# Kernel tuning notes

Measured on AMD Instinct MI355X. Metric: run time of the kernel, lower is better.

The kernel has to match this reference:

```python
import jax, jax.numpy as jnp
import numpy as np

N_NODES = 100000
N_EDGES = 1600000
IN_CH, HID, EMB = 128, 64, 32


def _glorot(key, shape):
    lim = np.sqrt(6.0 / (shape[0] + shape[1])).astype(np.float32)
    return jax.random.uniform(key, shape, jnp.float32, -lim, lim)


def setup_inputs() -> dict:
    key = jax.random.key(0)
    ks = jax.random.split(key, 5)
    x = jax.random.normal(ks[0], (N_NODES, IN_CH), dtype=jnp.float32)
    edges = jax.random.randint(ks[1], (2, N_EDGES), 0, N_NODES)
    W1 = _glorot(ks[2], (IN_CH, HID)); b1 = jnp.zeros((HID,), jnp.float32)
    W2 = _glorot(ks[3], (HID, EMB)); b2 = jnp.zeros((EMB,), jnp.float32)
    W3 = _glorot(ks[4], (HID, EMB)); b3 = jnp.zeros((EMB,), jnp.float32)
    return {"x": x, "edges": edges, "W1": W1, "b1": b1,
            "W2": W2, "b2": b2, "W3": W3, "b3": b3}


def reference(x, edges, W1, b1, W2, b2, W3, b3):
    N = x.shape[0]
    # GCNConv default: add self-loops, symmetric D^-1/2 A D^-1/2 normalization
    loop = jnp.arange(N, dtype=edges.dtype)
    src = jnp.concatenate([edges[0], loop])  # [E+N] message sources
    dst = jnp.concatenate([edges[1], loop])  # [E+N] message targets
    deg = jax.ops.segment_sum(jnp.ones_like(dst, dtype=x.dtype), dst, num_segments=N)
    dinv = jnp.where(deg > 0, jax.lax.rsqrt(deg), 0.0)
    norm = dinv[src] * dinv[dst]  # [E+N], cached across the three convs (cached=True)

    def gcn(h, W, b):
        h = h @ W                                  # [N, out]
        msg = h[src] * norm[:, None]               # gather + edge scale
        return jax.ops.segment_sum(msg, dst, num_segments=N) + b  # scatter-add

    h = jax.nn.relu(gcn(x, W1, b1))
    return gcn(h, W2, b2), gcn(h, W3, b3)
```

## Files before the change

kernel.cpp:

```cpp
#include <hip/hip_runtime.h>

#define NN 100000
#define NE 1600000
#define NB 391
#define CHUNK 4096
#define NCHUNK 391

__device__ inline unsigned short f2bf(float f) {
    unsigned int u = __float_as_uint(f);
    unsigned int r = u + 0x7fffu + ((u >> 16) & 1u);
    return (unsigned short)(r >> 16);
}
__device__ inline float bf_lo(unsigned int u) { return __uint_as_float(u << 16); }
__device__ inline float bf_hi(unsigned int u) { return __uint_as_float(u & 0xffff0000u); }

__global__ __launch_bounds__(256) void k_hist(const int* __restrict__ dst,
                                              int* __restrict__ bhist) {
    __shared__ int lh[NB];
    int t = threadIdx.x;
    for (int i = t; i < NB; i += 256) lh[i] = 0;
    __syncthreads();
    for (int e = blockIdx.x * 256 + t; e < NE; e += 256 * 256)
        atomicAdd(&lh[dst[e] >> 8], 1);
    __syncthreads();
    for (int i = t; i < NB; i += 256)
        if (lh[i]) atomicAdd(&bhist[i], lh[i]);
}

__global__ __launch_bounds__(256) void k_scanb(const int* __restrict__ bhist,
                                               int* __restrict__ boff,
                                               int* __restrict__ bcur) {
    __shared__ int sh[256];
    int t = threadIdx.x;
    int base = t * 2;
    int v0 = (base + 0 < NB) ? bhist[base + 0] : 0;
    int v1 = (base + 1 < NB) ? bhist[base + 1] : 0;
    int tsum = v0 + v1;
    sh[t] = tsum;
    __syncthreads();
    for (int d = 1; d < 256; d <<= 1) {
        int x = (t >= d) ? sh[t - d] : 0;
        __syncthreads();
        sh[t] += x;
        __syncthreads();
    }
    int excl = sh[t] - tsum;
    if (base + 0 < NB) { boff[base + 0] = excl;      bcur[base + 0] = excl; }
    if (base + 1 < NB) { boff[base + 1] = excl + v0; bcur[base + 1] = excl + v0; }
    if (t == 255) boff[NB] = sh[255];
}

__global__ __launch_bounds__(512) void k_bscatter(const int* __restrict__ src,
                                                  const int* __restrict__ dst,
                                                  int* __restrict__ bcur,
                                                  unsigned int* __restrict__ pairs) {
    __shared__ int lh[NB];
    __shared__ int lbase[NB];
    int t = threadIdx.x;
    int e0 = blockIdx.x * CHUNK;
    int e1 = min(e0 + CHUNK, NE);
    for (int i = t; i < NB; i += 512) lh[i] = 0;
    __syncthreads();
    for (int e = e0 + t; e < e1; e += 512)
        atomicAdd(&lh[dst[e] >> 8], 1);
    __syncthreads();
    int rot = (int)((blockIdx.x * 97u) % NB);
    for (int i = t; i < NB; i += 512) {
        int ii = i + rot; if (ii >= NB) ii -= NB;
        int h = lh[ii];
        lbase[ii] = h ? atomicAdd(&bcur[ii], h) : 0;
    }
    __syncthreads();
    for (int i = t; i < NB; i += 512) lh[i] = 0;
    __syncthreads();
    for (int e = e0 + t; e < e1; e += 512) {
        int d = dst[e];
        int b = d >> 8;
        int r = atomicAdd(&lh[b], 1);
        pairs[lbase[b] + r] = (unsigned int)src[e] | ((unsigned int)(d & 255) << 17);
    }
}

__global__ __launch_bounds__(256) void k_fine(const unsigned int* __restrict__ pairs,
                                              const int* __restrict__ boff,
                                              int* __restrict__ csr_off,
                                              int* __restrict__ csr_src,
                                              float* __restrict__ dinv) {
    __shared__ int lcnt[256];
    __shared__ int sc[256];
    __shared__ int lofs[256];
    int t = threadIdx.x;
    int b = blockIdx.x;
    int n0 = b << 8;
    int nnode = min(256, NN - n0);
    int bO = boff[b], bE = boff[b + 1];

    lcnt[t] = 0;
    __syncthreads();
    for (int e = bO + t; e < bE; e += 256)
        atomicAdd(&lcnt[pairs[e] >> 17], 1);
    __syncthreads();
    sc[t] = lcnt[t];
    __syncthreads();
    for (int d = 1; d < 256; d <<= 1) {
        int x = (t >= d) ? sc[t - d] : 0;
        __syncthreads();
        sc[t] += x;
        __syncthreads();
    }
    {
        int excl = sc[t] - lcnt[t];
        lofs[t] = excl;
        if (t < nnode) {
            int n = n0 + t;
            csr_off[n] = bO + excl;
            dinv[n] = rsqrtf(1.0f + (float)lcnt[t]);
        }
        lcnt[t] = 0;
    }
    if (b == NB - 1 && t == 0) csr_off[NN] = NE;
    __syncthreads();
    for (int e = bO + t; e < bE; e += 256) {
        unsigned int w = pairs[e];
        int li = (int)(w >> 17);
        int r = atomicAdd(&lcnt[li], 1);
        csr_src[bO + lofs[li] + r] = (int)(w & 0x1FFFFu);
    }
}

__global__ __launch_bounds__(256) void k_gemm1(const float* __restrict__ x,
                                               const float* __restrict__ W1,
                                               const float* __restrict__ dinv,
                                               unsigned short* __restrict__ t1b) {
    __shared__ float xs[64][132];
    __shared__ float ws[128 * 64];
    const int t = threadIdx.x;
    const int row0 = blockIdx.x * 64;
    const int nrows = min(64, NN - row0);

    #pragma unroll
    for (int i = 0; i < 8; ++i) {
        int f = t + i * 256;
        *(float4*)&ws[f * 4] = ((const float4*)W1)[f];
    }
    #pragma unroll
    for (int i = 0; i < 8; ++i) {
        int f = t + i * 256;
        int r = f >> 5, k4 = f & 31;
        float4 v = make_float4(0.f, 0.f, 0.f, 0.f);
        if (r < nrows) v = ((const float4*)(x + (size_t)(row0 + r) * 128))[k4];
        *(float4*)&xs[r][k4 * 4] = v;
    }
    __syncthreads();

    const int tc = t & 15;
    const int tr = t >> 4;
    float acc[4][4];
    #pragma unroll
    for (int i = 0; i < 4; ++i)
        #pragma unroll
        for (int j = 0; j < 4; ++j) acc[i][j] = 0.f;

    #pragma unroll 4
    for (int k = 0; k < 128; ++k) {
        float4 wv = *(const float4*)&ws[k * 64 + tc * 4];
        #pragma unroll
        for (int i = 0; i < 4; ++i) {
            float xv = xs[tr * 4 + i][k];
            acc[i][0] += xv * wv.x; acc[i][1] += xv * wv.y;
            acc[i][2] += xv * wv.z; acc[i][3] += xv * wv.w;
        }
    }
    #pragma unroll
    for (int i = 0; i < 4; ++i) {
        int r = tr * 4 + i;
        if (r < nrows) {
            float dn = dinv[row0 + r];
            ushort4 o;
            o.x = f2bf(acc[i][0] * dn); o.y = f2bf(acc[i][1] * dn);
            o.z = f2bf(acc[i][2] * dn); o.w = f2bf(acc[i][3] * dn);
            *(ushort4*)&t1b[(size_t)(row0 + r) * 64 + tc * 4] = o;
        }
    }
}

template <bool RELU>
__global__ __launch_bounds__(256) void k_gather8(const int* __restrict__ off,
                                                 const int* __restrict__ csr,
                                                 const float* __restrict__ dinv,
                                                 const unsigned short* __restrict__ hb,
                                                 const float* __restrict__ bias,
                                                 unsigned int* __restrict__ outp) {
    int idx = blockIdx.x * 256 + threadIdx.x;
    int n = idx >> 3;
    if (n >= NN) return;
    int c8 = idx & 7;
    const uint4* h4 = (const uint4*)hb;
    float dn = dinv[n];
    float acc[8];
    {
        uint4 v = h4[(size_t)n * 8 + c8];
        acc[0] = bf_lo(v.x); acc[1] = bf_hi(v.x);
        acc[2] = bf_lo(v.y); acc[3] = bf_hi(v.y);
        acc[4] = bf_lo(v.z); acc[5] = bf_hi(v.z);
        acc[6] = bf_lo(v.w); acc[7] = bf_hi(v.w);
    }
    int b = off[n], e = off[n + 1];
    int i = b;
    if (i < e) {
        int s = csr[i];
        for (++i; i < e; ++i) {
            int sn = csr[i];
            uint4 v = h4[(size_t)s * 8 + c8];
            acc[0] += bf_lo(v.x); acc[1] += bf_hi(v.x);
            acc[2] += bf_lo(v.y); acc[3] += bf_hi(v.y);
            acc[4] += bf_lo(v.z); acc[5] += bf_hi(v.z);
            acc[6] += bf_lo(v.w); acc[7] += bf_hi(v.w);
            s = sn;
        }
        uint4 v = h4[(size_t)s * 8 + c8];
        acc[0] += bf_lo(v.x); acc[1] += bf_hi(v.x);
        acc[2] += bf_lo(v.y); acc[3] += bf_hi(v.y);
        acc[4] += bf_lo(v.z); acc[5] += bf_hi(v.z);
        acc[6] += bf_lo(v.w); acc[7] += bf_hi(v.w);
    }
    float o[8];
    if (RELU) {
        float4 b0 = ((const float4*)bias)[c8 * 2];
        float4 b1 = ((const float4*)bias)[c8 * 2 + 1];
        o[0] = dn * fmaxf(dn * acc[0] + b0.x, 0.f);
        o[1] = dn * fmaxf(dn * acc[1] + b0.y, 0.f);
        o[2] = dn * fmaxf(dn * acc[2] + b0.z, 0.f);
        o[3] = dn * fmaxf(dn * acc[3] + b0.w, 0.f);
        o[4] = dn * fmaxf(dn * acc[4] + b1.x, 0.f);
        o[5] = dn * fmaxf(dn * acc[5] + b1.y, 0.f);
        o[6] = dn * fmaxf(dn * acc[6] + b1.z, 0.f);
        o[7] = dn * fmaxf(dn * acc[7] + b1.w, 0.f);
    } else {
        #pragma unroll
        for (int j = 0; j < 8; ++j) o[j] = dn * acc[j];
    }
    uint4 p;
    p.x = (unsigned int)f2bf(o[0]) | ((unsigned int)f2bf(o[1]) << 16);
    p.y = (unsigned int)f2bf(o[2]) | ((unsigned int)f2bf(o[3]) << 16);
    p.z = (unsigned int)f2bf(o[4]) | ((unsigned int)f2bf(o[5]) << 16);
    p.w = (unsigned int)f2bf(o[6]) | ((unsigned int)f2bf(o[7]) << 16);
    ((uint4*)outp)[(size_t)n * 8 + c8] = p;
}

__global__ __launch_bounds__(256) void k_gemm2(const unsigned short* __restrict__ aggb,
                                               const float* __restrict__ W2, const float* __restrict__ b2,
                                               const float* __restrict__ W3, const float* __restrict__ b3,
                                               float* __restrict__ out) {
    __shared__ float as_[64][72];
    __shared__ float wc[64 * 64];
    __shared__ float bc[64];
    const int t = threadIdx.x;
    const int row0 = blockIdx.x * 64;
    const int nrows = min(64, NN - row0);

    #pragma unroll
    for (int i = 0; i < 16; ++i) {
        int f = t + i * 256;
        int k = f >> 6, c = f & 63;
        wc[f] = (c < 32) ? W2[k * 32 + c] : W3[k * 32 + (c - 32)];
    }
    if (t < 64) bc[t] = (t < 32) ? b2[t] : b3[t - 32];
    #pragma unroll
    for (int i = 0; i < 2; ++i) {
        int f = t + i * 256;
        int r = f >> 3, c8 = f & 7;
        uint4 v = make_uint4(0u, 0u, 0u, 0u);
        if (r < nrows) v = ((const uint4*)(aggb + (size_t)(row0 + r) * 64))[c8];
        float* dp = &as_[r][c8 * 8];
        dp[0] = bf_lo(v.x); dp[1] = bf_hi(v.x);
        dp[2] = bf_lo(v.y); dp[3] = bf_hi(v.y);
        dp[4] = bf_lo(v.z); dp[5] = bf_hi(v.z);
        dp[6] = bf_lo(v.w); dp[7] = bf_hi(v.w);
    }
    __syncthreads();

    const int tc = t & 15;
    const int tr = t >> 4;
    float acc[4][4];
    #pragma unroll
    for (int i = 0; i < 4; ++i)
        #pragma unroll
        for (int j = 0; j < 4; ++j) acc[i][j] = 0.f;

    #pragma unroll 4
    for (int k = 0; k < 64; ++k) {
        float4 wv = *(const float4*)&wc[k * 64 + tc * 4];
        #pragma unroll
        for (int i = 0; i < 4; ++i) {
            float xv = as_[tr * 4 + i][k];
            acc[i][0] += xv * wv.x; acc[i][1] += xv * wv.y;
            acc[i][2] += xv * wv.z; acc[i][3] += xv * wv.w;
        }
    }
    const int c0 = tc * 4;
    float4 bias = *(float4*)&bc[c0];
    #pragma unroll
    for (int i = 0; i < 4; ++i) {
        int r = tr * 4 + i;
        if (r < nrows) {
            float4 o = make_float4(acc[i][0] + bias.x, acc[i][1] + bias.y,
                                   acc[i][2] + bias.z, acc[i][3] + bias.w);
            size_t row = (size_t)(row0 + r);
            float* p = (tc < 8) ? (out + row * 32 + c0)
                                : (out + (size_t)NN * 32 + row * 32 + (c0 - 32));
            *(float4*)p = o;
        }
    }
}

extern "C" void kernel_launch(void* const* d_in, const int* in_sizes, int n_in,
                              void* d_out, int out_size, void* d_ws, size_t ws_size,
                              hipStream_t stream) {
    const float* x  = (const float*)d_in[0];
    const int* edges = (const int*)d_in[1];
    const float* W1 = (const float*)d_in[2];
    const float* b1 = (const float*)d_in[3];
    const float* W2 = (const float*)d_in[4];
    const float* b2 = (const float*)d_in[5];
    const float* W3 = (const float*)d_in[6];
    const float* b3 = (const float*)d_in[7];
    float* out = (float*)d_out;

    const int* srcs = edges;
    const int* dsts = edges + NE;

    int*   csr_off = (int*)d_ws;
    float* dinv    = (float*)((int*)d_ws + 100004);
    int*   csr_src = (int*)d_ws + 200004;
    int*   bhist   = (int*)d_ws + 1800004;
    int*   boff    = (int*)d_ws + 1800396;
    int*   bcur    = (int*)d_ws + 1800788;
    unsigned int*   pairs = (unsigned int*)((int*)d_ws + 1801184);
    unsigned short* t1b   = (unsigned short*)pairs;
    unsigned short* aggb  = (unsigned short*)pairs;
    unsigned short* h1b   = (unsigned short*)((int*)d_ws + 5001184);

    dim3 blk(256);
    const int gN8 = (NN * 8 + 255) / 256;
    const int gT = (NN + 63) / 64;

    hipMemsetAsync(bhist, 0, NB * sizeof(int), stream);
    k_hist<<<256, blk, 0, stream>>>(dsts, bhist);
    k_scanb<<<1, blk, 0, stream>>>(bhist, boff, bcur);
    k_bscatter<<<NCHUNK, dim3(512), 0, stream>>>(srcs, dsts, bcur, pairs);
    k_fine<<<NB, blk, 0, stream>>>(pairs, boff, csr_off, csr_src, dinv);

    k_gemm1<<<gT, blk, 0, stream>>>(x, W1, dinv, t1b);
    k_gather8<true><<<gN8, blk, 0, stream>>>(csr_off, csr_src, dinv, t1b, b1,
                                             (unsigned int*)h1b);
    k_gather8<false><<<gN8, blk, 0, stream>>>(csr_off, csr_src, dinv, h1b, b1,
                                              (unsigned int*)aggb);
    k_gemm2<<<gT, blk, 0, stream>>>(aggb, W2, b2, W3, b3, out);
}
```

Measured before the change: 180.4 us.

## Use bf16 MFMA for the first-layer GEMM with pre-transposed bf16 weights

Replaces the FP32 scalar FMA tiled GEMM in the first GCN layer with MFMA 16x16x32 bf16 instructions. A small new kernel converts W1 to bf16 and transposes it, and x is rounded to bf16 while it is staged into LDS. This cuts the LDS footprint and moves the arithmetic onto the matrix cores. In exchange, inputs and weights lose precision before the multiply, and the output stores become scattered 2-byte writes instead of ushort4 vectors.

Result: faster. 162.4 us (-10.0%).

```diff
diff --git a/kernel.cpp b/kernel.cpp
--- a/kernel.cpp
+++ b/kernel.cpp
@@ -5,6 +5,9 @@
 #define NB 391
 #define CHUNK 4096
 #define NCHUNK 391
+
+typedef __attribute__((ext_vector_type(8))) short short8_t;
+typedef __attribute__((ext_vector_type(4))) float float4_t;
 
 __device__ inline unsigned short f2bf(float f) {
     unsigned int u = __float_as_uint(f);
@@ -128,12 +131,20 @@
     }
 }
 
+__global__ __launch_bounds__(256) void k_w1t(const float* __restrict__ W1,
+                                             unsigned short* __restrict__ wtb) {
+    int f = blockIdx.x * 256 + threadIdx.x;
+    int c = f >> 7, k = f & 127;
+    wtb[f] = f2bf(W1[k * 64 + c]);
+}
+
 __global__ __launch_bounds__(256) void k_gemm1(const float* __restrict__ x,
-                                               const float* __restrict__ W1,
+                                               const unsigned short* __restrict__ wtb,
                                                const float* __restrict__ dinv,
                                                unsigned short* __restrict__ t1b) {
-    __shared__ float xs[64][132];
-    __shared__ float ws[128 * 64];
+    __shared__ __align__(16) unsigned short lx[64 * 136];
+    __shared__ __align__(16) unsigned short lw[64 * 136];
+    __shared__ float sdinv[64];
     const int t = threadIdx.x;
     const int row0 = blockIdx.x * 64;
     const int nrows = min(64, NN - row0);
@@ -141,45 +152,51 @@
     #pragma unroll
     for (int i = 0; i < 8; ++i) {
         int f = t + i * 256;
-        *(float4*)&ws[f * 4] = ((const float4*)W1)[f];
-    }
-    #pragma unroll
-    for (int i = 0; i < 8; ++i) {
+        int r = f >> 5, c4 = f & 31;
+        float4 v = make_float4(0.f, 0.f, 0.f, 0.f);
+        if (r < nrows) v = ((const float4*)(x + (size_t)(row0 + r) * 128))[c4];
+        ushort4 o;
+        o.x = f2bf(v.x); o.y = f2bf(v.y); o.z = f2bf(v.z); o.w = f2bf(v.w);
+        *(ushort4*)&lx[r * 136 + c4 * 4] = o;
+    }
+    #pragma unroll
+    for (int i = 0; i < 4; ++i) {
         int f = t + i * 256;
-        int r = f >> 5, k4 = f & 31;
-        float4 v = make_float4(0.f, 0.f, 0.f, 0.f);
-        if (r < nrows) v = ((const float4*)(x + (size_t)(row0 + r) * 128))[k4];
-        *(float4*)&xs[r][k4 * 4] = v;
-    }
-    __syncthreads();
-
-    const int tc = t & 15;
-    const int tr = t >> 4;
-    float acc[4][4];
-    #pragma unroll
-    for (int i = 0; i < 4; ++i)
+        int c = f >> 4, c8 = f & 15;
+        uint4 v = ((const uint4*)wtb)[f];
+        *(uint4*)&lw[c * 136 + c8 * 8] = v;
+    }
+    if (t < 64) sdinv[t] = (row0 + t < NN) ? dinv[row0 + t] : 0.f;
+    __syncthreads();
+
+    const int w = t >> 6, l = t & 63;
+    const int m15 = l & 15, kg = l >> 4;
+    const unsigned short* pa = &lx[(w * 16 + m15) * 136 + kg * 8];
+    const unsigned short* pb = &lw[m15 * 136 + kg * 8];
+
+    float4_t acc[4];
+    #pragma unroll
+    for (int cb = 0; cb < 4; ++cb) acc[cb] = (float4_t){0.f, 0.f, 0.f, 0.f};
+
+    #pragma unroll
+    for (int ks = 0; ks < 4; ++ks) {
+        short8_t a = *(const short8_t*)(pa + ks * 32);
         #pragma unroll
-        for (int j = 0; j < 4; ++j) acc[i][j] = 0.f;
-
-    #pragma unroll 4
-    for (int k = 0; k < 128; ++k) {
-        float4 wv = *(const float4*)&ws[k * 64 + tc * 4];
-        #pragma unroll
-        for (int i = 0; i < 4; ++i) {
-            float xv = xs[tr * 4 + i][k];
-            acc[i][0] += xv * wv.x; acc[i][1] += xv * wv.y;
-            acc[i][2] += xv * wv.z; acc[i][3] += xv * wv.w;
-        }
-    }
-    #pragma unroll
-    for (int i = 0; i < 4; ++i) {
-        int r = tr * 4 + i;
-        if (r < nrows) {
-            float dn = dinv[row0 + r];
-            ushort4 o;
-            o.x = f2bf(acc[i][0] * dn); o.y = f2bf(acc[i][1] * dn);
-            o.z = f2bf(acc[i][2] * dn); o.w = f2bf(acc[i][3] * dn);
-            *(ushort4*)&t1b[(size_t)(row0 + r) * 64 + tc * 4] = o;
+        for (int cb = 0; cb < 4; ++cb) {
+            short8_t b = *(const short8_t*)(pb + cb * (16 * 136) + ks * 32);
+            acc[cb] = __builtin_amdgcn_mfma_f32_16x16x32_bf16(a, b, acc[cb], 0, 0, 0);
+        }
+    }
+
+    #pragma unroll
+    for (int r = 0; r < 4; ++r) {
+        int lrow = w * 16 + kg * 4 + r;
+        if (lrow < nrows) {
+            float dn = sdinv[lrow];
+            size_t grow = (size_t)(row0 + lrow);
+            #pragma unroll
+            for (int cb = 0; cb < 4; ++cb)
+                t1b[grow * 64 + cb * 16 + m15] = f2bf(acc[cb][r] * dn);
         }
     }
 }
@@ -336,10 +353,11 @@
     int*   bhist   = (int*)d_ws + 1800004;
     int*   boff    = (int*)d_ws + 1800396;
     int*   bcur    = (int*)d_ws + 1800788;
-    unsigned int*   pairs = (unsigned int*)((int*)d_ws + 1801184);
+    unsigned short* wtb = (unsigned short*)((int*)d_ws + 1801184);
+    unsigned int*   pairs = (unsigned int*)((int*)d_ws + 1805280);
     unsigned short* t1b   = (unsigned short*)pairs;
     unsigned short* aggb  = (unsigned short*)pairs;
-    unsigned short* h1b   = (unsigned short*)((int*)d_ws + 5001184);
+    unsigned short* h1b   = (unsigned short*)((int*)d_ws + 5005280);
 
     dim3 blk(256);
     const int gN8 = (NN * 8 + 255) / 256;
@@ -347,11 +365,12 @@
 
     hipMemsetAsync(bhist, 0, NB * sizeof(int), stream);
     k_hist<<<256, blk, 0, stream>>>(dsts, bhist);
+    k_w1t<<<32, blk, 0, stream>>>(W1, wtb);
     k_scanb<<<1, blk, 0, stream>>>(bhist, boff, bcur);
     k_bscatter<<<NCHUNK, dim3(512), 0, stream>>>(srcs, dsts, bcur, pairs);
     k_fine<<<NB, blk, 0, stream>>>(pairs, boff, csr_off, csr_src, dinv);
 
-    k_gemm1<<<gT, blk, 0, stream>>>(x, W1, dinv, t1b);
+    k_gemm1<<<gT, blk, 0, stream>>>(x, wtb, dinv, t1b);
     k_gather8<true><<<gN8, blk, 0, stream>>>(csr_off, csr_src, dinv, t1b, b1,
                                              (unsigned int*)h1b);
     k_gather8<false><<<gN8, blk, 0, stream>>>(csr_off, csr_src, dinv, h1b, b1,
```
